# Kernel tuning notes

Hardware: AMD Instinct MI355X
Metric: run time of the kernel (lower is better)

## Reference

```python
import jax, jax.numpy as jnp
import numpy as np

B, N, D_MODEL, D_EDGE, H = 4, 256, 256, 64, 8
C = D_MODEL // H  # 32


def setup_inputs() -> dict:
    key = jax.random.key(0)
    ks = jax.random.split(key, 10)
    w = lambda k, sh: (jax.random.normal(k, sh, jnp.float32) * 0.02)
    return {
        "x": jax.random.normal(ks[0], (B, N, D_MODEL), jnp.float32),
        "edge_attr": jax.random.normal(ks[1], (B, N, N, D_EDGE), jnp.float32),
        "attn_mask": jax.random.randint(ks[2], (B, N, N), 0, 2).astype(bool),
        "W_q": w(ks[3], (D_MODEL, D_MODEL)), "b_q": jnp.zeros((D_MODEL,), jnp.float32),
        "W_k": w(ks[4], (D_MODEL, D_MODEL)), "b_k": jnp.zeros((D_MODEL,), jnp.float32),
        "W_v": w(ks[5], (D_MODEL, D_MODEL)), "b_v": jnp.zeros((D_MODEL,), jnp.float32),
        "W_e": w(ks[6], (D_EDGE, D_MODEL)),  # lin_edge has no bias
        "W_s": w(ks[7], (D_MODEL, D_MODEL)), "b_s": jnp.zeros((D_MODEL,), jnp.float32),
    }


def reference(x, edge_attr, attn_mask, W_q, b_q, W_k, b_k, W_v, b_v, W_e, W_s, b_s):
    # x: (B,N,D); edge_attr: (B,N,N,DE); attn_mask: (B,N,N) bool
    b, n, d = x.shape
    scale = 1.0 / np.sqrt(C).astype(np.float32)
    Q = (x @ W_q + b_q).reshape(b, n, H, C)
    K = (x @ W_k + b_k).reshape(b, n, H, C)
    V = (x @ W_v + b_v).reshape(b, n, H, C)
    E = (edge_attr @ W_e).reshape(b, n, n, H, C)  # per-edge K/V bias
    # alpha_ij = Q_i . (K_j + E_ij) / sqrt(C)  -> split into QK + QE (same math)
    scores = (jnp.einsum("bihc,bjhc->bijh", Q, K)
              + jnp.einsum("bihc,bijhc->bijh", Q, E)) * scale
    scores = jnp.where(attn_mask[..., None], scores, -jnp.inf)
    alpha = jax.nn.softmax(scores, axis=2)           # softmax over source nodes j
    alpha = jnp.nan_to_num(alpha, nan=0.0)           # fully-masked rows -> 0
    # out_i = sum_j alpha_ij * (V_j + E_ij)   (dropout is identity in eval)
    out = (jnp.einsum("bijh,bjhc->bihc", alpha, V)
           + jnp.einsum("bijh,bijhc->bihc", alpha, E)).reshape(b, n, d)
    return out + x @ W_s + b_s
```

## Files before the change

### kernel.cpp

```cpp
#include <hip/hip_runtime.h>

#define NBATCH 4
#define NN 256
#define DM 256
#define DEDGE 64
#define NHEAD 8
#define CDIM 32

#define OQ  0
#define OK  262144
#define OV  524288
#define OS  786432
#define OWT 1048576

static __device__ __forceinline__ float4 ld4(const float* p) {
    return *reinterpret_cast<const float4*>(p);
}

__global__ __launch_bounds__(256) void fused_qkvs(
    const float* __restrict__ x,
    const float* __restrict__ Wq, const float* __restrict__ bq,
    const float* __restrict__ Wk, const float* __restrict__ bk,
    const float* __restrict__ Wv, const float* __restrict__ bv,
    const float* __restrict__ Wsk, const float* __restrict__ bsk,
    const float* __restrict__ We, float* __restrict__ ws)
{
    const int t = threadIdx.x;
    const int bid = blockIdx.x;

    if (bid == 256) {
        #pragma unroll
        for (int k = 0; k < 64; ++k) {
            int o = k * 256 + t;
            ws[OWT + o] = We[(o & 63) * 256 + (o >> 6)];
        }
        return;
    }

    __shared__ float xs[16 * 256];

    const int tile = bid & 63;
    const int mat  = bid >> 6;
    const float* W; const float* bb; float* out;
    if      (mat == 0) { W = Wq;  bb = bq;  out = ws + OQ; }
    else if (mat == 1) { W = Wk;  bb = bk;  out = ws + OK; }
    else if (mat == 2) { W = Wv;  bb = bv;  out = ws + OV; }
    else               { W = Wsk; bb = bsk; out = ws + OS; }

    const int r0 = tile * 16;
    {
        const float4* xsrc = reinterpret_cast<const float4*>(x + r0 * 256);
        float4* xd = reinterpret_cast<float4*>(xs);
        #pragma unroll
        for (int k = 0; k < 4; ++k) xd[t + k * 256] = xsrc[t + k * 256];
    }
    __syncthreads();

    const int c4 = (t & 63) * 4;
    const int rg = t >> 6;
    float acc[4][4] = {};

    #pragma unroll 4
    for (int d = 0; d < 256; ++d) {
        float4 wv = ld4(&W[d * 256 + c4]);
        #pragma unroll
        for (int rr = 0; rr < 4; ++rr) {
            float xv = xs[(rg * 4 + rr) * 256 + d];
            acc[rr][0] += xv * wv.x; acc[rr][1] += xv * wv.y;
            acc[rr][2] += xv * wv.z; acc[rr][3] += xv * wv.w;
        }
    }

    float4 bv4 = ld4(&bb[c4]);
    #pragma unroll
    for (int rr = 0; rr < 4; ++rr) {
        float4 o;
        o.x = acc[rr][0] + bv4.x; o.y = acc[rr][1] + bv4.y;
        o.z = acc[rr][2] + bv4.z; o.w = acc[rr][3] + bv4.w;
        *reinterpret_cast<float4*>(&out[(r0 + rg * 4 + rr) * 256 + c4]) = o;
    }
}

__global__ __launch_bounds__(256) void fused_attn(
    const float* __restrict__ edge, const unsigned char* __restrict__ mask,
    const float* __restrict__ We, const float* __restrict__ ws,
    float* __restrict__ out)
{
    __shared__ float qs[256];
    __shared__ float Ps[512];
    __shared__ float pt[8 * 260];
    __shared__ float As[512];
    __shared__ float mx[8];
    __shared__ float sm[8];
    __shared__ int mflag;

    const float* Q  = ws + OQ;
    const float* K  = ws + OK;
    const float* V  = ws + OV;
    const float* SK = ws + OS;
    const float* WT = ws + OWT;

    const int t   = threadIdx.x;
    const int row = blockIdx.x;
    const int b   = row >> 8;
    const float* erow = edge + (size_t)row * (NN * DEDGE);

    if (t == 0) mflag = 0;
    __syncthreads();

    {
        int found = 0;
        #pragma unroll
        for (int k = 0; k < 16; ++k)
            if ((k & 3) != 0 && mask[t * 16 + k]) found = 1;
        if (found) mflag = 1;
    }

    qs[t] = Q[row * 256 + t];
    __syncthreads();

    const bool mk = mflag ? (mask[row * 256 + t] != 0)
                          : (reinterpret_cast<const int*>(mask)[row * 256 + t] != 0);

    #pragma unroll
    for (int rep = 0; rep < 2; ++rep) {
        int idx = t + rep * 256;
        int h = idx >> 6, d = idx & 63;
        float a = 0.f;
        #pragma unroll
        for (int c = 0; c < 32; ++c) a += qs[h * 32 + c] * WT[(h * 32 + c) * 64 + d];
        Ps[idx] = a;
    }
    __syncthreads();

    float s[8];
    {
        const float* krow = K + ((b << 8) | t) * 256;
        #pragma unroll
        for (int h = 0; h < 8; ++h) {
            float a = 0.f;
            #pragma unroll
            for (int c = 0; c < 32; c += 4) {
                float4 kv = ld4(&krow[h * 32 + c]);
                float4 qv = ld4(&qs[h * 32 + c]);
                a += qv.x * kv.x + qv.y * kv.y + qv.z * kv.z + qv.w * kv.w;
            }
            s[h] = a;
        }
        #pragma unroll
        for (int k = 0; k < 16; ++k) {
            float4 ev = ld4(&erow[t * 64 + k * 4]);
            #pragma unroll
            for (int h = 0; h < 8; ++h) {
                float4 pv = ld4(&Ps[h * 64 + k * 4]);
                s[h] += ev.x * pv.x + ev.y * pv.y + ev.z * pv.z + ev.w * pv.w;
            }
        }
        const float scale = 0.17677669529663687f;
        #pragma unroll
        for (int h = 0; h < 8; ++h) {
            s[h] *= scale;
            if (!mk) s[h] = -1e30f;
            pt[h * 260 + t] = s[h];
        }
    }
    __syncthreads();

    {
        int h = t >> 5, l = t & 31;
        float m = -1e30f;
        #pragma unroll
        for (int k = 0; k < 8; ++k) m = fmaxf(m, pt[h * 260 + l + k * 32]);
        #pragma unroll
        for (int off = 16; off; off >>= 1) m = fmaxf(m, __shfl_xor(m, off));
        if (l == 0) mx[h] = m;
    }
    __syncthreads();

    float p[8];
    #pragma unroll
    for (int h = 0; h < 8; ++h) {
        p[h] = mk ? __expf(s[h] - mx[h]) : 0.f;
        pt[h * 260 + t] = p[h];
    }
    __syncthreads();

    {
        int h = t >> 5, l = t & 31;
        float a = 0.f;
        #pragma unroll
        for (int k = 0; k < 8; ++k) a += pt[h * 260 + l + k * 32];
        #pragma unroll
        for (int off = 16; off; off >>= 1) a += __shfl_xor(a, off);
        if (l == 0) sm[h] = a;
    }
    __syncthreads();

    float accV = 0.f;
    {
        int h = t >> 5;
        const float* vcol = V + (b << 8) * 256 + t;
        #pragma unroll 4
        for (int j4 = 0; j4 < 64; ++j4) {
            float4 pv = ld4(&pt[h * 260 + j4 * 4]);
            accV += pv.x * vcol[(j4 * 4 + 0) * 256];
            accV += pv.y * vcol[(j4 * 4 + 1) * 256];
            accV += pv.z * vcol[(j4 * 4 + 2) * 256];
            accV += pv.w * vcol[(j4 * 4 + 3) * 256];
        }
    }

    {
        int h2 = t >> 6, d = t & 63;
        float a0 = 0.f, a1 = 0.f;
        #pragma unroll 4
        for (int j4 = 0; j4 < 64; ++j4) {
            float4 p0 = ld4(&pt[h2 * 260 + j4 * 4]);
            float4 p1 = ld4(&pt[(h2 + 4) * 260 + j4 * 4]);
            float e0 = erow[(j4 * 4 + 0) * 64 + d];
            float e1 = erow[(j4 * 4 + 1) * 64 + d];
            float e2 = erow[(j4 * 4 + 2) * 64 + d];
            float e3 = erow[(j4 * 4 + 3) * 64 + d];
            a0 += p0.x * e0 + p0.y * e1 + p0.z * e2 + p0.w * e3;
            a1 += p1.x * e0 + p1.y * e1 + p1.z * e2 + p1.w * e3;
        }
        As[h2 * 64 + d] = a0;
        As[(h2 + 4) * 64 + d] = a1;
    }
    __syncthreads();

    {
        int h = t >> 5;
        float accE = 0.f;
        #pragma unroll
        for (int d4 = 0; d4 < 16; ++d4) {
            float4 av = ld4(&As[h * 64 + d4 * 4]);
            accE += av.x * We[(d4 * 4 + 0) * 256 + t];
            accE += av.y * We[(d4 * 4 + 1) * 256 + t];
            accE += av.z * We[(d4 * 4 + 2) * 256 + t];
            accE += av.w * We[(d4 * 4 + 3) * 256 + t];
        }
        float denom = sm[h];
        float inv = denom > 0.f ? 1.f / denom : 0.f;
        out[row * 256 + t] = (accV + accE) * inv + SK[row * 256 + t];
    }
}

extern "C" void kernel_launch(void* const* d_in, const int* in_sizes, int n_in,
                              void* d_out, int out_size, void* d_ws, size_t ws_size,
                              hipStream_t stream) {
    const float* x    = (const float*)d_in[0];
    const float* edge = (const float*)d_in[1];
    const unsigned char* mask = (const unsigned char*)d_in[2];
    const float* Wq = (const float*)d_in[3];
    const float* bq = (const float*)d_in[4];
    const float* Wk = (const float*)d_in[5];
    const float* bk = (const float*)d_in[6];
    const float* Wv = (const float*)d_in[7];
    const float* bv = (const float*)d_in[8];
    const float* We = (const float*)d_in[9];
    const float* Wsk = (const float*)d_in[10];
    const float* bsk = (const float*)d_in[11];
    float* out = (float*)d_out;
    float* ws  = (float*)d_ws;

    fused_qkvs<<<257, 256, 0, stream>>>(x, Wq, bq, Wk, bk, Wv, bv, Wsk, bsk, We, ws);
    fused_attn<<<1024, 256, 0, stream>>>(edge, mask, We, ws, out);
}
```

Baseline: 212.0 us.

## Stage edge tiles in swizzled LDS, transpose K, and split projection GEMM finer

The score phase now loads 64-row edge chunks into XOR-swizzled shared memory and has each thread compute two heads for one source node, instead of one thread per node striding 256-byte rows in global memory. K is stored transposed by the projection kernel so QK reads coalesce. The projection kernel uses four times as many blocks, each producing 16x64 outputs. Accumulators are split into independent partial sums to shorten dependency chains. The cost is extra barriers per chunk, 16KB more LDS per block, and redundant x tile loads across column blocks.

```diff
diff --git a/kernel.cpp b/kernel.cpp
--- a/kernel.cpp
+++ b/kernel.cpp
@@ -1,11 +1,4 @@
 #include <hip/hip_runtime.h>
-
-#define NBATCH 4
-#define NN 256
-#define DM 256
-#define DEDGE 64
-#define NHEAD 8
-#define CDIM 32
 
 #define OQ  0
 #define OK  262144
@@ -28,7 +21,7 @@
     const int t = threadIdx.x;
     const int bid = blockIdx.x;
 
-    if (bid == 256) {
+    if (bid == 1024) {
         #pragma unroll
         for (int k = 0; k < 64; ++k) {
             int o = k * 256 + t;
@@ -38,16 +31,18 @@
     }
 
     __shared__ float xs[16 * 256];
-
-    const int tile = bid & 63;
-    const int mat  = bid >> 6;
-    const float* W; const float* bb; float* out;
-    if      (mat == 0) { W = Wq;  bb = bq;  out = ws + OQ; }
-    else if (mat == 1) { W = Wk;  bb = bk;  out = ws + OK; }
-    else if (mat == 2) { W = Wv;  bb = bv;  out = ws + OV; }
-    else               { W = Wsk; bb = bsk; out = ws + OS; }
-
-    const int r0 = tile * 16;
+    __shared__ float xp[64 * 17];
+
+    const int mat = bid >> 8;
+    const int sub = bid & 255;
+    const int r0 = (sub >> 2) * 16;
+    const int c0 = (sub & 3) * 64;
+    const float* W; const float* bb;
+    if      (mat == 0) { W = Wq;  bb = bq;  }
+    else if (mat == 1) { W = Wk;  bb = bk;  }
+    else if (mat == 2) { W = Wv;  bb = bv;  }
+    else               { W = Wsk; bb = bsk; }
+
     {
         const float4* xsrc = reinterpret_cast<const float4*>(x + r0 * 256);
         float4* xd = reinterpret_cast<float4*>(xs);
@@ -56,28 +51,36 @@
     }
     __syncthreads();
 
-    const int c4 = (t & 63) * 4;
-    const int rg = t >> 6;
-    float acc[4][4] = {};
-
-    #pragma unroll 4
+    const int tr = t >> 4;
+    const int tc = t & 15;
+    float a0 = 0.f, a1 = 0.f, a2 = 0.f, a3 = 0.f;
+    #pragma unroll 8
     for (int d = 0; d < 256; ++d) {
-        float4 wv = ld4(&W[d * 256 + c4]);
-        #pragma unroll
-        for (int rr = 0; rr < 4; ++rr) {
-            float xv = xs[(rg * 4 + rr) * 256 + d];
-            acc[rr][0] += xv * wv.x; acc[rr][1] += xv * wv.y;
-            acc[rr][2] += xv * wv.z; acc[rr][3] += xv * wv.w;
-        }
-    }
-
-    float4 bv4 = ld4(&bb[c4]);
-    #pragma unroll
-    for (int rr = 0; rr < 4; ++rr) {
-        float4 o;
-        o.x = acc[rr][0] + bv4.x; o.y = acc[rr][1] + bv4.y;
-        o.z = acc[rr][2] + bv4.z; o.w = acc[rr][3] + bv4.w;
-        *reinterpret_cast<float4*>(&out[(r0 + rg * 4 + rr) * 256 + c4]) = o;
+        float4 wv = ld4(&W[d * 256 + c0 + tc * 4]);
+        float xv = xs[tr * 256 + d];
+        a0 += xv * wv.x; a1 += xv * wv.y; a2 += xv * wv.z; a3 += xv * wv.w;
+    }
+    float4 bv4 = ld4(&bb[c0 + tc * 4]);
+    a0 += bv4.x; a1 += bv4.y; a2 += bv4.z; a3 += bv4.w;
+
+    if (mat != 1) {
+        float* outp = ws + (mat == 0 ? OQ : (mat == 2 ? OV : OS));
+        float4 o = make_float4(a0, a1, a2, a3);
+        *reinterpret_cast<float4*>(&outp[(r0 + tr) * 256 + c0 + tc * 4]) = o;
+    } else {
+        xp[(tc * 4 + 0) * 17 + tr] = a0;
+        xp[(tc * 4 + 1) * 17 + tr] = a1;
+        xp[(tc * 4 + 2) * 17 + tr] = a2;
+        xp[(tc * 4 + 3) * 17 + tr] = a3;
+        __syncthreads();
+        const int b = r0 >> 8, rb0 = r0 & 255;
+        float* KT = ws + OK + b * 65536;
+        const int rl = t & 15;
+        #pragma unroll
+        for (int q2 = 0; q2 < 4; ++q2) {
+            int hcl = q2 * 16 + (t >> 4);
+            KT[(c0 + hcl) * 256 + rb0 + rl] = xp[hcl * 17 + rl];
+        }
     }
 }
 
@@ -88,6 +91,7 @@
 {
     __shared__ float qs[256];
     __shared__ float Ps[512];
+    __shared__ float es[64 * 64];
     __shared__ float pt[8 * 260];
     __shared__ float As[512];
     __shared__ float mx[8];
@@ -95,7 +99,7 @@
     __shared__ int mflag;
 
     const float* Q  = ws + OQ;
-    const float* K  = ws + OK;
+    const float* KT = ws + OK;
     const float* V  = ws + OV;
     const float* SK = ws + OS;
     const float* WT = ws + OWT;
@@ -103,11 +107,10 @@
     const int t   = threadIdx.x;
     const int row = blockIdx.x;
     const int b   = row >> 8;
-    const float* erow = edge + (size_t)row * (NN * DEDGE);
+    const float* erow = edge + (size_t)row * (256 * 64);
 
     if (t == 0) mflag = 0;
     __syncthreads();
-
     {
         int found = 0;
         #pragma unroll
@@ -115,56 +118,66 @@
             if ((k & 3) != 0 && mask[t * 16 + k]) found = 1;
         if (found) mflag = 1;
     }
-
     qs[t] = Q[row * 256 + t];
     __syncthreads();
-
-    const bool mk = mflag ? (mask[row * 256 + t] != 0)
-                          : (reinterpret_cast<const int*>(mask)[row * 256 + t] != 0);
+    const int MB = mflag;
 
     #pragma unroll
     for (int rep = 0; rep < 2; ++rep) {
         int idx = t + rep * 256;
         int h = idx >> 6, d = idx & 63;
-        float a = 0.f;
-        #pragma unroll
-        for (int c = 0; c < 32; ++c) a += qs[h * 32 + c] * WT[(h * 32 + c) * 64 + d];
-        Ps[idx] = a;
-    }
-    __syncthreads();
-
-    float s[8];
-    {
-        const float* krow = K + ((b << 8) | t) * 256;
-        #pragma unroll
-        for (int h = 0; h < 8; ++h) {
-            float a = 0.f;
+        float pa = 0.f, pb = 0.f;
+        #pragma unroll
+        for (int c = 0; c < 32; c += 2) {
+            pa += qs[h * 32 + c]     * WT[(h * 32 + c) * 64 + d];
+            pb += qs[h * 32 + c + 1] * WT[(h * 32 + c + 1) * 64 + d];
+        }
+        Ps[idx] = pa + pb;
+    }
+    __syncthreads();
+
+    const int jl = t & 63;
+    const int hp = t >> 6;
+    const int h0 = 2 * hp, h1 = 2 * hp + 1;
+    const float scale = 0.17677669529663687f;
+
+    for (int c4 = 0; c4 < 4; ++c4) {
+        {
+            const float4* src = reinterpret_cast<const float4*>(erow + c4 * 4096);
             #pragma unroll
-            for (int c = 0; c < 32; c += 4) {
-                float4 kv = ld4(&krow[h * 32 + c]);
-                float4 qv = ld4(&qs[h * 32 + c]);
-                a += qv.x * kv.x + qv.y * kv.y + qv.z * kv.z + qv.w * kv.w;
+            for (int m = 0; m < 4; ++m) {
+                int q = m * 256 + t;
+                int r = q >> 4, k = q & 15;
+                *reinterpret_cast<float4*>(&es[r * 64 + ((k ^ (r & 15)) * 4)]) = src[q];
             }
-            s[h] = a;
-        }
+        }
+        __syncthreads();
+
+        const int j = c4 * 64 + jl;
+        float sa0 = 0.f, sb0 = 0.f, sa1 = 0.f, sb1 = 0.f;
         #pragma unroll
         for (int k = 0; k < 16; ++k) {
-            float4 ev = ld4(&erow[t * 64 + k * 4]);
-            #pragma unroll
-            for (int h = 0; h < 8; ++h) {
-                float4 pv = ld4(&Ps[h * 64 + k * 4]);
-                s[h] += ev.x * pv.x + ev.y * pv.y + ev.z * pv.z + ev.w * pv.w;
-            }
-        }
-        const float scale = 0.17677669529663687f;
-        #pragma unroll
-        for (int h = 0; h < 8; ++h) {
-            s[h] *= scale;
-            if (!mk) s[h] = -1e30f;
-            pt[h * 260 + t] = s[h];
-        }
-    }
-    __syncthreads();
+            float4 ev = ld4(&es[jl * 64 + ((k ^ (jl & 15)) * 4)]);
+            float4 p0 = ld4(&Ps[h0 * 64 + k * 4]);
+            float4 p1 = ld4(&Ps[h1 * 64 + k * 4]);
+            sa0 += ev.x * p0.x + ev.y * p0.y; sb0 += ev.z * p0.z + ev.w * p0.w;
+            sa1 += ev.x * p1.x + ev.y * p1.y; sb1 += ev.z * p1.z + ev.w * p1.w;
+        }
+        const float* kt = KT + b * 65536 + j;
+        #pragma unroll 8
+        for (int c = 0; c < 32; ++c) {
+            sa0 += qs[h0 * 32 + c] * kt[(h0 * 32 + c) * 256];
+            sa1 += qs[h1 * 32 + c] * kt[(h1 * 32 + c) * 256];
+        }
+        float s0 = (sa0 + sb0) * scale;
+        float s1 = (sa1 + sb1) * scale;
+        bool mk = MB ? (mask[row * 256 + j] != 0)
+                     : (reinterpret_cast<const int*>(mask)[row * 256 + j] != 0);
+        if (!mk) { s0 = -1e30f; s1 = -1e30f; }
+        pt[h0 * 260 + j] = s0;
+        pt[h1 * 260 + j] = s1;
+        __syncthreads();
+    }
 
     {
         int h = t >> 5, l = t & 31;
@@ -177,11 +190,14 @@
     }
     __syncthreads();
 
-    float p[8];
-    #pragma unroll
-    for (int h = 0; h < 8; ++h) {
-        p[h] = mk ? __expf(s[h] - mx[h]) : 0.f;
-        pt[h * 260 + t] = p[h];
+    {
+        bool mkt = MB ? (mask[row * 256 + t] != 0)
+                      : (reinterpret_cast<const int*>(mask)[row * 256 + t] != 0);
+        #pragma unroll
+        for (int h = 0; h < 8; ++h) {
+            float s = pt[h * 260 + t];
+            pt[h * 260 + t] = mkt ? __expf(s - mx[h]) : 0.f;
+        }
     }
     __syncthreads();
 
@@ -196,23 +212,25 @@
     }
     __syncthreads();
 
-    float accV = 0.f;
+    float accV;
     {
         int h = t >> 5;
         const float* vcol = V + (b << 8) * 256 + t;
+        float v0 = 0.f, v1 = 0.f, v2 = 0.f, v3 = 0.f;
         #pragma unroll 4
         for (int j4 = 0; j4 < 64; ++j4) {
             float4 pv = ld4(&pt[h * 260 + j4 * 4]);
-            accV += pv.x * vcol[(j4 * 4 + 0) * 256];
-            accV += pv.y * vcol[(j4 * 4 + 1) * 256];
-            accV += pv.z * vcol[(j4 * 4 + 2) * 256];
-            accV += pv.w * vcol[(j4 * 4 + 3) * 256];
-        }
+            v0 += pv.x * vcol[(j4 * 4 + 0) * 256];
+            v1 += pv.y * vcol[(j4 * 4 + 1) * 256];
+            v2 += pv.z * vcol[(j4 * 4 + 2) * 256];
+            v3 += pv.w * vcol[(j4 * 4 + 3) * 256];
+        }
+        accV = (v0 + v1) + (v2 + v3);
     }
 
     {
         int h2 = t >> 6, d = t & 63;
-        float a0 = 0.f, a1 = 0.f;
+        float a00=0.f,a01=0.f,a02=0.f,a03=0.f,a10=0.f,a11=0.f,a12=0.f,a13=0.f;
         #pragma unroll 4
         for (int j4 = 0; j4 < 64; ++j4) {
             float4 p0 = ld4(&pt[h2 * 260 + j4 * 4]);
@@ -221,25 +239,26 @@
             float e1 = erow[(j4 * 4 + 1) * 64 + d];
             float e2 = erow[(j4 * 4 + 2) * 64 + d];
             float e3 = erow[(j4 * 4 + 3) * 64 + d];
-            a0 += p0.x * e0 + p0.y * e1 + p0.z * e2 + p0.w * e3;
-            a1 += p1.x * e0 + p1.y * e1 + p1.z * e2 + p1.w * e3;
-        }
-        As[h2 * 64 + d] = a0;
-        As[(h2 + 4) * 64 + d] = a1;
+            a00 += p0.x * e0; a01 += p0.y * e1; a02 += p0.z * e2; a03 += p0.w * e3;
+            a10 += p1.x * e0; a11 += p1.y * e1; a12 += p1.z * e2; a13 += p1.w * e3;
+        }
+        As[h2 * 64 + d]       = (a00 + a01) + (a02 + a03);
+        As[(h2 + 4) * 64 + d] = (a10 + a11) + (a12 + a13);
     }
     __syncthreads();
 
     {
         int h = t >> 5;
-        float accE = 0.f;
+        float e0 = 0.f, e1 = 0.f, e2 = 0.f, e3 = 0.f;
         #pragma unroll
         for (int d4 = 0; d4 < 16; ++d4) {
             float4 av = ld4(&As[h * 64 + d4 * 4]);
-            accE += av.x * We[(d4 * 4 + 0) * 256 + t];
-            accE += av.y * We[(d4 * 4 + 1) * 256 + t];
-            accE += av.z * We[(d4 * 4 + 2) * 256 + t];
-            accE += av.w * We[(d4 * 4 + 3) * 256 + t];
-        }
+            e0 += av.x * We[(d4 * 4 + 0) * 256 + t];
+            e1 += av.y * We[(d4 * 4 + 1) * 256 + t];
+            e2 += av.z * We[(d4 * 4 + 2) * 256 + t];
+            e3 += av.w * We[(d4 * 4 + 3) * 256 + t];
+        }
+        float accE = (e0 + e1) + (e2 + e3);
         float denom = sm[h];
         float inv = denom > 0.f ? 1.f / denom : 0.f;
         out[row * 256 + t] = (accV + accE) * inv + SK[row * 256 + t];
@@ -264,6 +283,6 @@
     float* out = (float*)d_out;
     float* ws  = (float*)d_ws;
 
-    fused_qkvs<<<257, 256, 0, stream>>>(x, Wq, bq, Wk, bk, Wv, bv, Wsk, bsk, We, ws);
+    fused_qkvs<<<1025, 256, 0, stream>>>(x, Wq, bq, Wk, bk, Wv, bv, Wsk, bsk, We, ws);
     fused_attn<<<1024, 256, 0, stream>>>(edge, mask, We, ws, out);
 }
```

Measured after the change: 235.3 us. 11.0% more time.
